# Optimization experiments

Hardware: AMD Instinct MI355X
Metric: run time of the kernel (lower is better)

The kernel has to match this reference:

```python
import jax, jax.numpy as jnp
import numpy as np

GRID_SIZE = 5
SPLINE_ORDER = 3
HIDDEN = 128
N = 131072
K = 256          # num_cluster
EPS = 1e-8       # torch.cosine_similarity eps
N_COEF = GRID_SIZE + SPLINE_ORDER  # 8 spline basis functions per input feature


def make_grid():
    # efficient-kan grid: grid_range [-1,1], extended by spline_order on each side
    h = 2.0 / GRID_SIZE
    g = jnp.arange(-SPLINE_ORDER, GRID_SIZE + SPLINE_ORDER + 1, dtype=jnp.float32) * h - 1.0
    return jnp.tile(g[None, :], (HIDDEN, 1))  # (in, grid_size + 2*order + 1) = (128, 12)


def b_splines(x, grid):
    # x: (N, in), grid: (in, G) -> bases: (N, in, grid_size + spline_order)
    xe = x[..., None]
    bases = ((xe >= grid[:, :-1]) & (xe < grid[:, 1:])).astype(x.dtype)
    for p in range(1, SPLINE_ORDER + 1):
        left = (xe - grid[:, :-(p + 1)]) / (grid[:, p:-1] - grid[:, :-(p + 1)])
        right = (grid[:, p + 1:] - xe) / (grid[:, p + 1:] - grid[:, 1:-p])
        bases = left * bases[..., :-1] + right * bases[..., 1:]
    return bases


def kan_linear(x, grid, base_w, spline_w, scaler):
    # efficient-kan KANLinear: base path + spline path
    base = jax.nn.silu(x) @ base_w.T                       # (N, out)
    sp = b_splines(x, grid)                                # (N, in, coef)
    sw = spline_w * scaler[..., None]                      # (out, in, coef)
    return base + jnp.einsum('nic,oic->no', sp, sw)


def setup_inputs() -> dict:
    key = jax.random.key(0)
    ks = jax.random.split(key, 9)
    s = 1.0 / np.sqrt(HIDDEN)
    return {
        'x': jax.random.normal(ks[0], (N, HIDDEN), jnp.float32),
        'prototypes': jax.random.normal(ks[1], (K, HIDDEN), jnp.float32),
        'grid': make_grid(),
        'base_w1': jax.random.normal(ks[2], (HIDDEN, HIDDEN), jnp.float32) * s,
        'spline_w1': jax.random.normal(ks[3], (HIDDEN, HIDDEN, N_COEF), jnp.float32) * 0.1,
        'scaler1': jax.random.normal(ks[4], (HIDDEN, HIDDEN), jnp.float32) * s + 1.0,
        'base_w2': jax.random.normal(ks[5], (HIDDEN, HIDDEN), jnp.float32) * s,
        'spline_w2': jax.random.normal(ks[6], (HIDDEN, HIDDEN, N_COEF), jnp.float32) * 0.1,
        'scaler2': jax.random.normal(ks[7], (HIDDEN, HIDDEN), jnp.float32) * s + 1.0,
    }


def reference(x, prototypes, grid, base_w1, spline_w1, scaler1, base_w2, spline_w2, scaler2):
    # KAN([128,128,128]) = two KANLinear layers
    h = kan_linear(x, grid, base_w1, spline_w1, scaler1)
    emb = kan_linear(h, grid, base_w2, spline_w2, scaler2)     # (N, 128)
    # cosine similarity to all prototypes = normalized matmul (same math as
    # the broadcasted torch.cosine_similarity, without the (N,K,H) intermediate)
    xn = emb / jnp.maximum(jnp.linalg.norm(emb, axis=-1, keepdims=True), EPS)
    pn = prototypes / jnp.maximum(jnp.linalg.norm(prototypes, axis=-1, keepdims=True), EPS)
    sim = xn @ pn.T                                            # (N, K)
    cluster_assignments = jnp.argmax(sim, axis=1)              # (N,)
    return emb, cluster_assignments
```

## Files before the change

kernel.cpp:

```cpp
#include <hip/hip_runtime.h>
#include <math.h>

typedef unsigned short u16;
typedef _Float16 f16;
typedef __attribute__((ext_vector_type(8))) _Float16 f16x8;
typedef __attribute__((ext_vector_type(2))) _Float16 f16x2;
typedef __attribute__((ext_vector_type(4))) float f32x4;

#define N_ROWS 131072
#define HID 128
#define WS_CH 8192
#define N_WCH 72
#define N_PCH 8

__device__ __forceinline__ void split8(const float* a8, f16x8& hv, f16x8& lv) {
    union { f16x8 v; f16x2 p[4]; } H, L;
    #pragma unroll
    for (int j = 0; j < 4; ++j) {
        float v0 = a8[2 * j], v1 = a8[2 * j + 1];
        float h0 = __builtin_bit_cast(float, __builtin_bit_cast(unsigned, v0) & 0xFFFFE000u);
        float h1 = __builtin_bit_cast(float, __builtin_bit_cast(unsigned, v1) & 0xFFFFE000u);
        H.p[j] = __builtin_bit_cast(f16x2, __builtin_amdgcn_cvt_pkrtz(v0, v1));
        L.p[j] = __builtin_bit_cast(f16x2, __builtin_amdgcn_cvt_pkrtz(v0 - h0, v1 - h1));
    }
    hv = H.v; lv = L.v;
}

__device__ __forceinline__ float silu1(float v) {
    return v * __builtin_amdgcn_rcpf(1.0f + __expf(-v));
}

__device__ __forceinline__ void spline8(float xv, float* a8) {
    float s  = (xv + 2.2f) * 2.5f;
    float tf = floorf(s);
    int   tt = (int)tf;
    bool valid = (tt >= 0) && (tt <= 10);
    float kt = (float)(tt - 3) * 0.4f - 1.0f;
    float u  = (xv - kt) * 2.5f;
    float u2 = u * u, u3 = u2 * u;
    float om = 1.0f - u;
    float b3 = u3 * (1.0f / 6.0f);
    float b2 = (-3.f * u3 + 3.f * u2 + 3.f * u + 1.f) * (1.0f / 6.0f);
    float b1 = (3.f * u3 - 6.f * u2 + 4.f) * (1.0f / 6.0f);
    float b0 = om * om * om * (1.0f / 6.0f);
    #pragma unroll
    for (int c = 0; c < 8; ++c) {
        int d = tt - c;
        float v = 0.f;
        v = (d == 0) ? b3 : v;
        v = (d == 1) ? b2 : v;
        v = (d == 2) ? b1 : v;
        v = (d == 3) ? b0 : v;
        a8[c] = valid ? v : 0.f;
    }
}

__device__ __forceinline__ int tswz(int r, int c) {
    return (r << 7) + ((((c >> 2) ^ r) & 31) << 2) + (c & 3);
}

__global__ __launch_bounds__(256)
void pack_weights(const float* __restrict__ bw1, const float* __restrict__ sw1,
                  const float* __restrict__ sc1,
                  const float* __restrict__ bw2, const float* __restrict__ sw2,
                  const float* __restrict__ sc2,
                  const float* __restrict__ protos, u16* __restrict__ ws)
{
    int gid = blockIdx.x * 256 + threadIdx.x;
    if (gid < N_WCH * 4096) {
        int l  = gid / (36 * 4096);
        int r  = gid % (36 * 4096);
        int ch = r / 4096;
        int e  = r % 4096;
        int o  = e >> 5;
        int kl = e & 31;
        const float* bw = l ? bw2 : bw1;
        const float* sw = l ? sw2 : sw1;
        const float* sc = l ? sc2 : sc1;
        float v;
        if (ch < 4) {
            v = bw[o * HID + ch * 32 + kl];
        } else {
            int i = (ch - 4) * 4 + (kl >> 3);
            v = sw[(o * HID + i) * 8 + (kl & 7)] * sc[o * HID + i];
        }
        f16 hi = (f16)v;
        f16 lo = (f16)(v - (float)hi);
        int nt = o >> 4, n = o & 15, kq = kl >> 3, c = kl & 7;
        size_t base = (size_t)(l * 36 + ch) * WS_CH;
        size_t idx  = ((size_t)nt * 64 + kq * 16 + n) * 8 + c;
        ws[base + idx]        = __builtin_bit_cast(u16, hi);
        ws[base + 4096 + idx] = __builtin_bit_cast(u16, lo);
    } else if (gid < (N_WCH + N_PCH) * 4096) {
        int r  = gid - N_WCH * 4096;
        int hk = r / 4096;
        int e  = r % 4096;
        int pl = e >> 5;
        int kl = e & 31;
        int half = hk >> 2, kc = hk & 3;
        int p = half * 128 + pl;
        const float4 pv = *(const float4*)(protos + (size_t)p * HID + kl * 4);
        float s = pv.x * pv.x + pv.y * pv.y + pv.z * pv.z + pv.w * pv.w;
        #pragma unroll
        for (int off = 1; off < 32; off <<= 1) s += __shfl_xor(s, off);
        float rp = 1.0f / fmaxf(sqrtf(s), 1e-8f);
        float v = protos[(size_t)p * HID + kc * 32 + kl] * rp;
        f16 hi = (f16)v;
        f16 lo = (f16)(v - (float)hi);
        int nt = pl >> 4, n = pl & 15, kq = kl >> 3, c = kl & 7;
        size_t base = (size_t)(N_WCH + hk) * WS_CH;
        size_t idx  = ((size_t)nt * 64 + kq * 16 + n) * 8 + c;
        ws[base + idx]        = __builtin_bit_cast(u16, hi);
        ws[base + 4096 + idx] = __builtin_bit_cast(u16, lo);
    }
}

__global__ __launch_bounds__(256, 2)
void kan_fused(const float* __restrict__ x, const u16* __restrict__ wpack,
               float* __restrict__ emb_out, float* __restrict__ assign_out)
{
    __shared__ float t[128 * 128];
    __shared__ u16   Bfrag[2][8][64][8];

    const int tid  = threadIdx.x;
    const int lane = tid & 63;
    const int w    = tid >> 6;
    const int m    = lane & 15;
    const int q    = lane >> 4;
    const int row0 = w * 32 + m;
    const int brow = blockIdx.x * 128;

    const char* gptr = (const char*)wpack + (size_t)w * 4096 + (size_t)lane * 16;
    uint4* const lptr = (uint4*)&Bfrag[0][0][0][0] + w * 256 + lane;
    uint4 rr0, rr1, rr2, rr3;

#define ISSUE_LOADS() do {                                                         \
        rr0 = *(const uint4*)(gptr);                                               \
        rr1 = *(const uint4*)(gptr + 1024);                                        \
        rr2 = *(const uint4*)(gptr + 2048);                                        \
        rr3 = *(const uint4*)(gptr + 3072);                                        \
        gptr += 16384;                                                             \
    } while (0)

#define STORE_LDS() do {                                                           \
        lptr[0] = rr0; lptr[64] = rr1; lptr[128] = rr2; lptr[192] = rr3;           \
    } while (0)

#define PIPE_BARRIER() do {                                                        \
        asm volatile("s_waitcnt lgkmcnt(0)" ::: "memory");                         \
        __builtin_amdgcn_s_barrier();                                              \
        __builtin_amdgcn_sched_barrier(0);                                         \
    } while (0)

    ISSUE_LOADS();

    {
        const int m2 = tid >> 1, hf = tid & 1;
        const float4* src = (const float4*)(x + (size_t)(brow + m2) * HID + hf * 64);
        #pragma unroll
        for (int j = 0; j < 16; ++j) {
            float4 v = src[j];
            *(float4*)&t[tswz(m2, hf * 64 + j * 4)] = v;
        }
    }

    struct ASet { f16x8 h0, l0, h1, l1; };
    ASet SA, SB;
    f32x4 acc0[8], acc1[8];

    auto bsync = [&](bool issue) {
        PIPE_BARRIER();
        STORE_LDS();
        if (issue) ISSUE_LOADS();
        PIPE_BARRIER();
    };

    auto zero_accs = [&]() {
        #pragma unroll
        for (int nt = 0; nt < 8; ++nt) {
            acc0[nt] = (f32x4){0.f, 0.f, 0.f, 0.f};
            acc1[nt] = (f32x4){0.f, 0.f, 0.f, 0.f};
        }
    };

    auto mfma48 = [&](const ASet& A) {
        #pragma unroll
        for (int nt = 0; nt < 8; ++nt) {
            f16x8 bhv = *(const f16x8*)Bfrag[0][nt][lane];
            f16x8 blv = *(const f16x8*)Bfrag[1][nt][lane];
            acc0[nt] = __builtin_amdgcn_mfma_f32_16x16x32_f16(A.h0, bhv, acc0[nt], 0, 0, 0);
            acc0[nt] = __builtin_amdgcn_mfma_f32_16x16x32_f16(A.l0, bhv, acc0[nt], 0, 0, 0);
            acc0[nt] = __builtin_amdgcn_mfma_f32_16x16x32_f16(A.h0, blv, acc0[nt], 0, 0, 0);
            acc1[nt] = __builtin_amdgcn_mfma_f32_16x16x32_f16(A.h1, bhv, acc1[nt], 0, 0, 0);
            acc1[nt] = __builtin_amdgcn_mfma_f32_16x16x32_f16(A.l1, bhv, acc1[nt], 0, 0, 0);
            acc1[nt] = __builtin_amdgcn_mfma_f32_16x16x32_f16(A.h1, blv, acc1[nt], 0, 0, 0);
        }
    };

    auto prep_silu = [&](int ch, ASet& N) {
        float a8[8];
        float4 u0 = *(const float4*)&t[tswz(row0, ch * 32 + q * 8)];
        float4 u1 = *(const float4*)&t[tswz(row0, ch * 32 + q * 8 + 4)];
        a8[0] = silu1(u0.x); a8[1] = silu1(u0.y); a8[2] = silu1(u0.z); a8[3] = silu1(u0.w);
        a8[4] = silu1(u1.x); a8[5] = silu1(u1.y); a8[6] = silu1(u1.z); a8[7] = silu1(u1.w);
        split8(a8, N.h0, N.l0);
        float4 v0 = *(const float4*)&t[tswz(row0 + 16, ch * 32 + q * 8)];
        float4 v1 = *(const float4*)&t[tswz(row0 + 16, ch * 32 + q * 8 + 4)];
        a8[0] = silu1(v0.x); a8[1] = silu1(v0.y); a8[2] = silu1(v0.z); a8[3] = silu1(v0.w);
        a8[4] = silu1(v1.x); a8[5] = silu1(v1.y); a8[6] = silu1(v1.z); a8[7] = silu1(v1.w);
        split8(a8, N.h1, N.l1);
    };
    auto prep_spline = [&](int ch, ASet& N) {
        float s0 = t[tswz(row0,      (ch - 4) * 4 + q)];
        float s1 = t[tswz(row0 + 16, (ch - 4) * 4 + q)];
        float a8[8];
        spline8(s0, a8); split8(a8, N.h0, N.l0);
        spline8(s1, a8); split8(a8, N.h1, N.l1);
    };
    auto prep_pass = [&](int kc, ASet& N) {
        float a8[8];
        float4 u0 = *(const float4*)&t[tswz(row0, kc * 32 + q * 8)];
        float4 u1 = *(const float4*)&t[tswz(row0, kc * 32 + q * 8 + 4)];
        a8[0] = u0.x; a8[1] = u0.y; a8[2] = u0.z; a8[3] = u0.w;
        a8[4] = u1.x; a8[5] = u1.y; a8[6] = u1.z; a8[7] = u1.w;
        split8(a8, N.h0, N.l0);
        float4 v0 = *(const float4*)&t[tswz(row0 + 16, kc * 32 + q * 8)];
        float4 v1 = *(const float4*)&t[tswz(row0 + 16, kc * 32 + q * 8 + 4)];
        a8[0] = v0.x; a8[1] = v0.y; a8[2] = v0.z; a8[3] = v0.w;
        a8[4] = v1.x; a8[5] = v1.y; a8[6] = v1.z; a8[7] = v1.w;
        split8(a8, N.h1, N.l1);
    };

    #define PRIO_ON()  __builtin_amdgcn_s_setprio(1)
    #define PRIO_OFF() __builtin_amdgcn_s_setprio(0)

    for (int l = 0; l < 2; ++l) {
        zero_accs();
        prep_silu(0, SA);
        bsync(true); PRIO_ON(); mfma48(SA); prep_silu(1, SB); PRIO_OFF();
        bsync(true); PRIO_ON(); mfma48(SB); prep_silu(2, SA); PRIO_OFF();
        bsync(true); PRIO_ON(); mfma48(SA); prep_silu(3, SB); PRIO_OFF();
        bsync(true); PRIO_ON(); mfma48(SB); prep_spline(4, SA); PRIO_OFF();
        for (int ch = 4; ch < 34; ch += 2) {
            bsync(true); PRIO_ON(); mfma48(SA); prep_spline(ch + 1, SB); PRIO_OFF();
            bsync(true); PRIO_ON(); mfma48(SB); prep_spline(ch + 2, SA); PRIO_OFF();
        }
        bsync(true); PRIO_ON(); mfma48(SA); prep_spline(35, SB); PRIO_OFF();
        bsync(true); PRIO_ON(); mfma48(SB); PRIO_OFF();

        #pragma unroll
        for (int nt = 0; nt < 8; ++nt)
            #pragma unroll
            for (int r = 0; r < 4; ++r) {
                t[tswz(w * 32 + q * 4 + r,      nt * 16 + m)] = acc0[nt][r];
                t[tswz(w * 32 + 16 + q * 4 + r, nt * 16 + m)] = acc1[nt][r];
            }
    }

    {
        const int m2 = tid >> 1, hf = tid & 1;
        float* dst = emb_out + (size_t)(brow + m2) * HID + hf * 64;
        #pragma unroll
        for (int j = 0; j < 16; ++j)
            *(float4*)(dst + j * 4) = *(const float4*)&t[tswz(m2, hf * 64 + j * 4)];
    }

    float best0[4], best1[4]; int bi0[4], bi1[4];
    #pragma unroll
    for (int r = 0; r < 4; ++r) {
        best0[r] = -3.402823466e+38f; bi0[r] = 0;
        best1[r] = -3.402823466e+38f; bi1[r] = 0;
    }

    auto reduce_half = [&](int half) {
        #pragma unroll
        for (int nt = 0; nt < 8; ++nt) {
            int p = half * 128 + nt * 16 + m;
            #pragma unroll
            for (int r = 0; r < 4; ++r) {
                float v0 = acc0[nt][r];
                if (v0 > best0[r]) { best0[r] = v0; bi0[r] = p; }
                float v1 = acc1[nt][r];
                if (v1 > best1[r]) { best1[r] = v1; bi1[r] = p; }
            }
            acc0[nt] = (f32x4){0.f, 0.f, 0.f, 0.f};
            acc1[nt] = (f32x4){0.f, 0.f, 0.f, 0.f};
        }
    };

    zero_accs();
    prep_pass(0, SA);
    bsync(true);  PRIO_ON(); mfma48(SA); prep_pass(1, SB); PRIO_OFF();
    bsync(true);  PRIO_ON(); mfma48(SB); prep_pass(2, SA); PRIO_OFF();
    bsync(true);  PRIO_ON(); mfma48(SA); prep_pass(3, SB); PRIO_OFF();
    bsync(true);  PRIO_ON(); mfma48(SB); prep_pass(0, SA); PRIO_OFF();
    reduce_half(0);
    bsync(true);  PRIO_ON(); mfma48(SA); prep_pass(1, SB); PRIO_OFF();
    bsync(true);  PRIO_ON(); mfma48(SB); prep_pass(2, SA); PRIO_OFF();
    bsync(true);  PRIO_ON(); mfma48(SA); prep_pass(3, SB); PRIO_OFF();
    bsync(false); PRIO_ON(); mfma48(SB); PRIO_OFF();
    reduce_half(1);

    #pragma unroll
    for (int r = 0; r < 4; ++r) {
        #pragma unroll
        for (int off = 1; off < 16; off <<= 1) {
            float ov0 = __shfl_xor(best0[r], off);
            int   oi0 = __shfl_xor(bi0[r], off);
            if (ov0 > best0[r] || (ov0 == best0[r] && oi0 < bi0[r])) { best0[r] = ov0; bi0[r] = oi0; }
            float ov1 = __shfl_xor(best1[r], off);
            int   oi1 = __shfl_xor(bi1[r], off);
            if (ov1 > best1[r] || (ov1 == best1[r] && oi1 < bi1[r])) { best1[r] = ov1; bi1[r] = oi1; }
        }
        if (m == 0) {
            assign_out[(size_t)brow + w * 32 + q * 4 + r]      = (float)bi0[r];
            assign_out[(size_t)brow + w * 32 + 16 + q * 4 + r] = (float)bi1[r];
        }
    }
#undef ISSUE_LOADS
#undef STORE_LDS
#undef PIPE_BARRIER
}

extern "C" void kernel_launch(void* const* d_in, const int* in_sizes, int n_in,
                              void* d_out, int out_size, void* d_ws, size_t ws_size,
                              hipStream_t stream) {
    (void)in_sizes; (void)n_in; (void)out_size; (void)ws_size;

    const float* x      = (const float*)d_in[0];
    const float* protos = (const float*)d_in[1];
    const float* bw1 = (const float*)d_in[3];
    const float* sw1 = (const float*)d_in[4];
    const float* sc1 = (const float*)d_in[5];
    const float* bw2 = (const float*)d_in[6];
    const float* sw2 = (const float*)d_in[7];
    const float* sc2 = (const float*)d_in[8];

    float* out    = (float*)d_out;
    float* embp   = out;
    float* assign = out + (size_t)N_ROWS * HID;
    u16*   wpack  = (u16*)d_ws;

    pack_weights<<<dim3((N_WCH + N_PCH) * 4096 / 256), dim3(256), 0, stream>>>(
        bw1, sw1, sc1, bw2, sw2, sc2, protos, wpack);
    kan_fused<<<dim3(N_ROWS / 128), dim3(256), 0, stream>>>(
        x, wpack, embp, assign);
}
```

Measured before the change: 390.7 us.

## Load B fragments directly from global into registers, drop LDS staging and barriers

Replaces the cooperative LDS-staged weight pipeline (a global load into registers, a store to shared Bfrag, and two barriers per chunk) with each wave loading its full B fragments (16 uint4 per chunk) straight from global/L2 into registers before its MFMAs. This removes the per-chunk block barriers and the LDS traffic for weights. In exchange each wave now reads four times as much weight data from the cache, register pressure rises, and the software double-buffering that overlapped the next chunk's load with the current MFMAs is gone, so load latency may be exposed unless the compiler hoists the loads.

```diff
diff --git a/kernel.cpp b/kernel.cpp
--- a/kernel.cpp
+++ b/kernel.cpp
@@ -120,7 +120,6 @@
                float* __restrict__ emb_out, float* __restrict__ assign_out)
 {
     __shared__ float t[128 * 128];
-    __shared__ u16   Bfrag[2][8][64][8];
 
     const int tid  = threadIdx.x;
     const int lane = tid & 63;
@@ -130,29 +129,7 @@
     const int row0 = w * 32 + m;
     const int brow = blockIdx.x * 128;
 
-    const char* gptr = (const char*)wpack + (size_t)w * 4096 + (size_t)lane * 16;
-    uint4* const lptr = (uint4*)&Bfrag[0][0][0][0] + w * 256 + lane;
-    uint4 rr0, rr1, rr2, rr3;
-
-#define ISSUE_LOADS() do {                                                         \
-        rr0 = *(const uint4*)(gptr);                                               \
-        rr1 = *(const uint4*)(gptr + 1024);                                        \
-        rr2 = *(const uint4*)(gptr + 2048);                                        \
-        rr3 = *(const uint4*)(gptr + 3072);                                        \
-        gptr += 16384;                                                             \
-    } while (0)
-
-#define STORE_LDS() do {                                                           \
-        lptr[0] = rr0; lptr[64] = rr1; lptr[128] = rr2; lptr[192] = rr3;           \
-    } while (0)
-
-#define PIPE_BARRIER() do {                                                        \
-        asm volatile("s_waitcnt lgkmcnt(0)" ::: "memory");                         \
-        __builtin_amdgcn_s_barrier();                                              \
-        __builtin_amdgcn_sched_barrier(0);                                         \
-    } while (0)
-
-    ISSUE_LOADS();
+    const char* const gB = (const char*)wpack + (size_t)lane * 16;
 
     {
         const int m2 = tid >> 1, hf = tid & 1;
@@ -164,15 +141,17 @@
         }
     }
 
-    struct ASet { f16x8 h0, l0, h1, l1; };
-    ASet SA, SB;
+    f16x8 ah0, al0, ah1, al1;
     f32x4 acc0[8], acc1[8];
-
-    auto bsync = [&](bool issue) {
-        PIPE_BARRIER();
-        STORE_LDS();
-        if (issue) ISSUE_LOADS();
-        PIPE_BARRIER();
+    uint4 bh[8], bl[8];
+
+    auto loadB = [&](int reg) {
+        const char* g = gB + (size_t)reg * 16384;
+        #pragma unroll
+        for (int nt = 0; nt < 8; ++nt) {
+            bh[nt] = *(const uint4*)(g + nt * 1024);
+            bl[nt] = *(const uint4*)(g + 8192 + nt * 1024);
+        }
     };
 
     auto zero_accs = [&]() {
@@ -183,71 +162,64 @@
         }
     };
 
-    auto mfma48 = [&](const ASet& A) {
+    auto mfma48 = [&]() {
+        __builtin_amdgcn_s_setprio(1);
         #pragma unroll
         for (int nt = 0; nt < 8; ++nt) {
-            f16x8 bhv = *(const f16x8*)Bfrag[0][nt][lane];
-            f16x8 blv = *(const f16x8*)Bfrag[1][nt][lane];
-            acc0[nt] = __builtin_amdgcn_mfma_f32_16x16x32_f16(A.h0, bhv, acc0[nt], 0, 0, 0);
-            acc0[nt] = __builtin_amdgcn_mfma_f32_16x16x32_f16(A.l0, bhv, acc0[nt], 0, 0, 0);
-            acc0[nt] = __builtin_amdgcn_mfma_f32_16x16x32_f16(A.h0, blv, acc0[nt], 0, 0, 0);
-            acc1[nt] = __builtin_amdgcn_mfma_f32_16x16x32_f16(A.h1, bhv, acc1[nt], 0, 0, 0);
-            acc1[nt] = __builtin_amdgcn_mfma_f32_16x16x32_f16(A.l1, bhv, acc1[nt], 0, 0, 0);
-            acc1[nt] = __builtin_amdgcn_mfma_f32_16x16x32_f16(A.h1, blv, acc1[nt], 0, 0, 0);
-        }
-    };
-
-    auto prep_silu = [&](int ch, ASet& N) {
+            f16x8 bhv = __builtin_bit_cast(f16x8, bh[nt]);
+            f16x8 blv = __builtin_bit_cast(f16x8, bl[nt]);
+            acc0[nt] = __builtin_amdgcn_mfma_f32_16x16x32_f16(ah0, bhv, acc0[nt], 0, 0, 0);
+            acc0[nt] = __builtin_amdgcn_mfma_f32_16x16x32_f16(al0, bhv, acc0[nt], 0, 0, 0);
+            acc0[nt] = __builtin_amdgcn_mfma_f32_16x16x32_f16(ah0, blv, acc0[nt], 0, 0, 0);
+            acc1[nt] = __builtin_amdgcn_mfma_f32_16x16x32_f16(ah1, bhv, acc1[nt], 0, 0, 0);
+            acc1[nt] = __builtin_amdgcn_mfma_f32_16x16x32_f16(al1, bhv, acc1[nt], 0, 0, 0);
+            acc1[nt] = __builtin_amdgcn_mfma_f32_16x16x32_f16(ah1, blv, acc1[nt], 0, 0, 0);
+        }
+        __builtin_amdgcn_s_setprio(0);
+    };
+
+    auto prep_silu = [&](int ch) {
         float a8[8];
         float4 u0 = *(const float4*)&t[tswz(row0, ch * 32 + q * 8)];
         float4 u1 = *(const float4*)&t[tswz(row0, ch * 32 + q * 8 + 4)];
         a8[0] = silu1(u0.x); a8[1] = silu1(u0.y); a8[2] = silu1(u0.z); a8[3] = silu1(u0.w);
         a8[4] = silu1(u1.x); a8[5] = silu1(u1.y); a8[6] = silu1(u1.z); a8[7] = silu1(u1.w);
-        split8(a8, N.h0, N.l0);
+        split8(a8, ah0, al0);
         float4 v0 = *(const float4*)&t[tswz(row0 + 16, ch * 32 + q * 8)];
         float4 v1 = *(const float4*)&t[tswz(row0 + 16, ch * 32 + q * 8 + 4)];
         a8[0] = silu1(v0.x); a8[1] = silu1(v0.y); a8[2] = silu1(v0.z); a8[3] = silu1(v0.w);
         a8[4] = silu1(v1.x); a8[5] = silu1(v1.y); a8[6] = silu1(v1.z); a8[7] = silu1(v1.w);
-        split8(a8, N.h1, N.l1);
-    };
-    auto prep_spline = [&](int ch, ASet& N) {
+        split8(a8, ah1, al1);
+    };
+    auto prep_spline = [&](int ch) {
         float s0 = t[tswz(row0,      (ch - 4) * 4 + q)];
         float s1 = t[tswz(row0 + 16, (ch - 4) * 4 + q)];
         float a8[8];
-        spline8(s0, a8); split8(a8, N.h0, N.l0);
-        spline8(s1, a8); split8(a8, N.h1, N.l1);
-    };
-    auto prep_pass = [&](int kc, ASet& N) {
+        spline8(s0, a8); split8(a8, ah0, al0);
+        spline8(s1, a8); split8(a8, ah1, al1);
+    };
+    auto prep_pass = [&](int kc) {
         float a8[8];
         float4 u0 = *(const float4*)&t[tswz(row0, kc * 32 + q * 8)];
         float4 u1 = *(const float4*)&t[tswz(row0, kc * 32 + q * 8 + 4)];
         a8[0] = u0.x; a8[1] = u0.y; a8[2] = u0.z; a8[3] = u0.w;
         a8[4] = u1.x; a8[5] = u1.y; a8[6] = u1.z; a8[7] = u1.w;
-        split8(a8, N.h0, N.l0);
+        split8(a8, ah0, al0);
         float4 v0 = *(const float4*)&t[tswz(row0 + 16, kc * 32 + q * 8)];
         float4 v1 = *(const float4*)&t[tswz(row0 + 16, kc * 32 + q * 8 + 4)];
         a8[0] = v0.x; a8[1] = v0.y; a8[2] = v0.z; a8[3] = v0.w;
         a8[4] = v1.x; a8[5] = v1.y; a8[6] = v1.z; a8[7] = v1.w;
-        split8(a8, N.h1, N.l1);
-    };
-
-    #define PRIO_ON()  __builtin_amdgcn_s_setprio(1)
-    #define PRIO_OFF() __builtin_amdgcn_s_setprio(0)
+        split8(a8, ah1, al1);
+    };
 
     for (int l = 0; l < 2; ++l) {
         zero_accs();
-        prep_silu(0, SA);
-        bsync(true); PRIO_ON(); mfma48(SA); prep_silu(1, SB); PRIO_OFF();
-        bsync(true); PRIO_ON(); mfma48(SB); prep_silu(2, SA); PRIO_OFF();
-        bsync(true); PRIO_ON(); mfma48(SA); prep_silu(3, SB); PRIO_OFF();
-        bsync(true); PRIO_ON(); mfma48(SB); prep_spline(4, SA); PRIO_OFF();
-        for (int ch = 4; ch < 34; ch += 2) {
-            bsync(true); PRIO_ON(); mfma48(SA); prep_spline(ch + 1, SB); PRIO_OFF();
-            bsync(true); PRIO_ON(); mfma48(SB); prep_spline(ch + 2, SA); PRIO_OFF();
-        }
-        bsync(true); PRIO_ON(); mfma48(SA); prep_spline(35, SB); PRIO_OFF();
-        bsync(true); PRIO_ON(); mfma48(SB); PRIO_OFF();
-
+        for (int ch = 0; ch < 36; ++ch) {
+            loadB(l * 36 + ch);
+            if (ch < 4) prep_silu(ch);
+            else        prep_spline(ch);
+            mfma48();
+        }
         #pragma unroll
         for (int nt = 0; nt < 8; ++nt)
             #pragma unroll
@@ -283,23 +255,18 @@
                 float v1 = acc1[nt][r];
                 if (v1 > best1[r]) { best1[r] = v1; bi1[r] = p; }
             }
-            acc0[nt] = (f32x4){0.f, 0.f, 0.f, 0.f};
-            acc1[nt] = (f32x4){0.f, 0.f, 0.f, 0.f};
-        }
-    };
-
-    zero_accs();
-    prep_pass(0, SA);
-    bsync(true);  PRIO_ON(); mfma48(SA); prep_pass(1, SB); PRIO_OFF();
-    bsync(true);  PRIO_ON(); mfma48(SB); prep_pass(2, SA); PRIO_OFF();
-    bsync(true);  PRIO_ON(); mfma48(SA); prep_pass(3, SB); PRIO_OFF();
-    bsync(true);  PRIO_ON(); mfma48(SB); prep_pass(0, SA); PRIO_OFF();
-    reduce_half(0);
-    bsync(true);  PRIO_ON(); mfma48(SA); prep_pass(1, SB); PRIO_OFF();
-    bsync(true);  PRIO_ON(); mfma48(SB); prep_pass(2, SA); PRIO_OFF();
-    bsync(true);  PRIO_ON(); mfma48(SA); prep_pass(3, SB); PRIO_OFF();
-    bsync(false); PRIO_ON(); mfma48(SB); PRIO_OFF();
-    reduce_half(1);
+        }
+    };
+
+    for (int half = 0; half < 2; ++half) {
+        zero_accs();
+        for (int kc = 0; kc < 4; ++kc) {
+            loadB(N_WCH + half * 4 + kc);
+            prep_pass(kc);
+            mfma48();
+        }
+        reduce_half(half);
+    }
 
     #pragma unroll
     for (int r = 0; r < 4; ++r) {
@@ -317,9 +284,6 @@
             assign_out[(size_t)brow + w * 32 + 16 + q * 4 + r] = (float)bi1[r];
         }
     }
-#undef ISSUE_LOADS
-#undef STORE_LDS
-#undef PIPE_BARRIER
 }
 
 extern "C" void kernel_launch(void* const* d_in, const int* in_sizes, int n_in,
```

Result: faster. 379.1 us (-3.0%).
